# Kernel optimization log

Measured on AMD Instinct MI355X. Metric: run time of the kernel, lower is better.

Reference implementation:

```python
import jax, jax.numpy as jnp
import numpy as np

N_HEAD = 16

def setup_inputs() -> dict:
    key = jax.random.key(0)
    ks = jax.random.split(key, 5)
    B, T, C = 4, 2048, 1024
    s = 0.02
    return {
        "x": jax.random.normal(ks[0], (B, T, C), dtype=jnp.float32),
        "W_attn": jax.random.normal(ks[1], (C, 3 * C), dtype=jnp.float32) * s,
        "b_attn": jax.random.normal(ks[2], (3 * C,), dtype=jnp.float32) * s,
        "W_proj": jax.random.normal(ks[3], (C, C), dtype=jnp.float32) * s,
        "b_proj": jax.random.normal(ks[4], (C,), dtype=jnp.float32) * s,
    }

def reference(x, W_attn, b_attn, W_proj, b_proj):
    B, T, C = x.shape
    H = N_HEAD
    D = C // H
    qkv = x @ W_attn + b_attn                      # [B,T,3C]
    q, k, v = jnp.split(qkv, 3, axis=2)
    # [B,H,T,D]
    q = q.reshape(B, T, H, D).transpose(0, 2, 1, 3)
    k = k.reshape(B, T, H, D).transpose(0, 2, 1, 3)
    v = v.reshape(B, T, H, D).transpose(0, 2, 1, 3)
    scale = 1.0 / jnp.sqrt(jnp.float32(D))
    att = jnp.einsum('bhqd,bhkd->bhqk', q, k) * scale
    causal = jnp.tril(jnp.ones((T, T), dtype=bool))
    att = jnp.where(causal[None, None], att, -jnp.inf)
    att = jax.nn.softmax(att, axis=-1)
    y = jnp.einsum('bhqk,bhkd->bhqd', att, v)       # [B,H,T,D]
    y = y.transpose(0, 2, 1, 3).reshape(B, T, C)
    return y @ W_proj + b_proj
```

## Files before the change

### kernel.cpp

```cpp
#include <hip/hip_runtime.h>

typedef unsigned short u16;
typedef unsigned int u32;
typedef __bf16 bf16x8 __attribute__((ext_vector_type(8)));
typedef short s16x4 __attribute__((ext_vector_type(4)));
typedef float f32x4 __attribute__((ext_vector_type(4)));

#define MFMA16(a,b,c) __builtin_amdgcn_mfma_f32_16x16x32_bf16((a),(b),(c),0,0,0)

#if defined(__has_builtin)
#if __has_builtin(__builtin_amdgcn_mfma_f32_16x16x16bf16_1k)
#define MFMA1K(a,b,c) __builtin_amdgcn_mfma_f32_16x16x16bf16_1k((a),(b),(c),0,0,0)
#endif
#endif
#ifndef MFMA1K
__device__ __forceinline__ f32x4 mfma1k_asm(s16x4 a, s16x4 b, f32x4 c) {
    f32x4 d;
    asm volatile("v_mfma_f32_16x16x16_bf16 %0, %1, %2, %3"
                 : "=v"(d) : "v"(a), "v"(b), "0"(c));
    return d;
}
#define MFMA1K(a,b,c) mfma1k_asm((a),(b),(c))
#endif

__device__ __forceinline__ float b2f(u16 u) {
    u32 v = ((u32)u) << 16;
    return __builtin_bit_cast(float, v);
}
__device__ __forceinline__ u16 f2b(float f) {
    u32 u = __builtin_bit_cast(u32, f);
    u = u + 0x7FFFu + ((u >> 16) & 1u);
    return (u16)(u >> 16);
}

__device__ __forceinline__ void gload_lds16(const u16* g, u16* l) {
    __builtin_amdgcn_global_load_lds(
        (__attribute__((address_space(1))) void*)g,
        (__attribute__((address_space(3))) void*)l, 16, 0, 0);
}

__device__ __forceinline__ uint4 load8_bf16(const void* base, size_t off, int f32m) {
    if (f32m) {
        const float* p = (const float*)base + off;
        float4 a = *(const float4*)p;
        float4 b = *(const float4*)(p + 4);
        union { u16 u[8]; uint4 v; } t;
        t.u[0] = f2b(a.x); t.u[1] = f2b(a.y); t.u[2] = f2b(a.z); t.u[3] = f2b(a.w);
        t.u[4] = f2b(b.x); t.u[5] = f2b(b.y); t.u[6] = f2b(b.z); t.u[7] = f2b(b.w);
        return t.v;
    }
    return *(const uint4*)((const u16*)base + off);
}

__device__ __forceinline__ int detect_f32(const u16* __restrict__ x) {
    __shared__ int cnt;
    if (threadIdx.x == 0) cnt = 0;
    __syncthreads();
    int my = ((x[2 * (threadIdx.x * 128)] >> 7) & 0xFF) >= 0x90;
    unsigned long long b = __ballot(my);
    if ((threadIdx.x & 63) == 0) atomicAdd(&cnt, (int)__popcll(b));
    __syncthreads();
    return cnt > 32;
}

__device__ __forceinline__ void transpose_tile(
    const void* __restrict__ src, u16* __restrict__ dst, int R, int Cc,
    int f32m, int bx, int by)
{
    __shared__ u16 tile[64 * 72];
    const int t = threadIdx.x;
    const int c0 = bx * 64, r0 = by * 64;
    #pragma unroll
    for (int i = 0; i < 2; ++i) {
        int ch = t + 256 * i;
        int r = ch >> 3, c8 = (ch & 7) * 8;
        *(uint4*)&tile[r * 72 + c8] =
            load8_bf16(src, (size_t)(r0 + r) * Cc + c0 + c8, f32m);
    }
    __syncthreads();
    #pragma unroll
    for (int i = 0; i < 2; ++i) {
        int ch = t + 256 * i;
        int r = ch >> 3, c8 = (ch & 7) * 8;
        union { u16 u[8]; uint4 v; } tmp;
        #pragma unroll
        for (int j = 0; j < 8; ++j) tmp.u[j] = tile[(c8 + j) * 72 + r];
        *(uint4*)&dst[(size_t)(c0 + r) * R + r0 + c8] = tmp.v;
    }
}

__global__ __launch_bounds__(256) void k_prep(
    const u16* __restrict__ x, const void* __restrict__ Wa,
    const void* __restrict__ ba, const void* __restrict__ Wp,
    const void* __restrict__ bp,
    u16* __restrict__ WaT, u16* __restrict__ WpT, u16* __restrict__ Abf,
    u16* __restrict__ bac, u16* __restrict__ bpc, int* __restrict__ flag)
{
    const int f32m = detect_f32(x);
    int task = blockIdx.x;
    if (task < 768) {
        transpose_tile(Wa, WaT, 1024, 3072, f32m, task % 48, task / 48);
        return;
    }
    task -= 768;
    if (task < 256) {
        transpose_tile(Wp, WpT, 1024, 1024, f32m, task % 16, task / 16);
        return;
    }
    task -= 256;
    if (task < 4096) {
        if (!f32m) return;
        size_t i = ((size_t)task * 256 + threadIdx.x) * 8;
        const float* xf = (const float*)x;
        float4 a = *(const float4*)(xf + i);
        float4 b = *(const float4*)(xf + i + 4);
        union { u16 u[8]; uint4 v; } t;
        t.u[0] = f2b(a.x); t.u[1] = f2b(a.y); t.u[2] = f2b(a.z); t.u[3] = f2b(a.w);
        t.u[4] = f2b(b.x); t.u[5] = f2b(b.y); t.u[6] = f2b(b.z); t.u[7] = f2b(b.w);
        *(uint4*)(Abf + i) = t.v;
        return;
    }
    const int t = threadIdx.x;
    #pragma unroll
    for (int j = 0; j < 12; ++j) {
        int i = t + 256 * j;
        if (i < 3072) bac[i] = f32m ? f2b(((const float*)ba)[i]) : ((const u16*)ba)[i];
    }
    #pragma unroll
    for (int j = 0; j < 4; ++j) {
        int i = t + 256 * j;
        if (i < 1024) bpc[i] = f32m ? f2b(((const float*)bp)[i]) : ((const u16*)bp)[i];
    }
    if (t == 0) *flag = f32m;
}

__global__ __launch_bounds__(256) void k_gemm_qkv(
    const void* __restrict__ x, const u16* __restrict__ Abf,
    const u16* __restrict__ Bt, const u16* __restrict__ bias,
    const int* __restrict__ flag,
    u16* __restrict__ Ql, u16* __restrict__ Kl, u16* __restrict__ Vl)
{
    constexpr int K = 1024;
    __shared__ __align__(16) u16 As[128 * 64];
    __shared__ __align__(16) u16 Bs[128 * 64];
    const int t = threadIdx.x;
    const int lane = t & 63, w = t >> 6;
    const int quad = lane >> 4, m16 = lane & 15;
    const int wm = (w >> 1) * 64, wn = (w & 1) * 64;
    const int m0 = blockIdx.x * 128, n0 = blockIdx.y * 128;
    const int lr = lane >> 3;
    const int lc = (lane & 7) * 8;
    const u16* A = (*flag) ? Abf : (const u16*)x;

    const f32x4 z = {0.f, 0.f, 0.f, 0.f};
    f32x4 acc[4][4];
    #pragma unroll
    for (int mi = 0; mi < 4; ++mi)
        #pragma unroll
        for (int ni = 0; ni < 4; ++ni) acc[mi][ni] = z;

    for (int k0 = 0; k0 < K; k0 += 64) {
        __syncthreads();
        #pragma unroll
        for (int i = 0; i < 4; ++i) {
            const int chunk = w * 4 + i;
            const int row = chunk * 8 + lr;
            gload_lds16(&A [(size_t)(m0 + row) * K + k0 + lc], &As[chunk * 512]);
            gload_lds16(&Bt[(size_t)(n0 + row) * K + k0 + lc], &Bs[chunk * 512]);
        }
        __syncthreads();
        #pragma unroll
        for (int kk = 0; kk < 2; ++kk) {
            bf16x8 af[4], bfr[4];
            #pragma unroll
            for (int mi = 0; mi < 4; ++mi)
                af[mi] = *(const bf16x8*)&As[(wm + mi * 16 + m16) * 64 + kk * 32 + quad * 8];
            #pragma unroll
            for (int ni = 0; ni < 4; ++ni)
                bfr[ni] = *(const bf16x8*)&Bs[(wn + ni * 16 + m16) * 64 + kk * 32 + quad * 8];
            #pragma unroll
            for (int mi = 0; mi < 4; ++mi)
                #pragma unroll
                for (int ni = 0; ni < 4; ++ni)
                    acc[mi][ni] = MFMA16(af[mi], bfr[ni], acc[mi][ni]);
        }
    }

    const int sec = n0 >> 10;
    const float qscale = (sec == 0) ? 0.18033688011112042f : 1.0f;
    u16* Outp = (sec == 0) ? Ql : (sec == 1) ? Kl : Vl;
    #pragma unroll
    for (int mi = 0; mi < 4; ++mi) {
        #pragma unroll
        for (int ni = 0; ni < 4; ++ni) {
            int gn = n0 + wn + ni * 16 + m16;
            int sn = gn & 1023;
            int h = sn >> 6, d = sn & 63;
            float bv = b2f(bias[gn]);
            #pragma unroll
            for (int v = 0; v < 4; ++v) {
                int gm = m0 + wm + mi * 16 + quad * 4 + v;
                int bb = gm >> 11, tt = gm & 2047;
                u16 o = f2b((acc[mi][ni][v] + bv) * qscale);
                size_t bh = (size_t)(bb * 16 + h);
                Outp[(bh * 2048 + tt) * 64 + d] = o;
            }
        }
    }
}

__global__ __launch_bounds__(256) void k_attn(
    u16* __restrict__ Ql, const u16* __restrict__ Kl, const u16* __restrict__ Vl)
{
    __shared__ u16 Ks[128 * 80];
    __shared__ u16 Vs[64 * 132];
    const int t = threadIdx.x;
    const int lane = t & 63, w = t >> 6;
    const int quad = lane >> 4, m16 = lane & 15;
    const int g = blockIdx.x >> 6;
    const int p = g >> 2, r = g & 3;
    const int qb = (p == 0) ? 15 - r : (p == 1) ? 8 + r : (p == 2) ? 7 - r : r;
    const int bh = blockIdx.x & 63;
    const int q0 = qb * 128;

    bf16x8 fq[2][2];
    #pragma unroll
    for (int s = 0; s < 2; ++s) {
        const u16* Qp = Ql + ((size_t)bh * 2048 + q0 + s * 64 + w * 16 + m16) * 64;
        fq[s][0] = *(const bf16x8*)&Qp[quad * 8];
        fq[s][1] = *(const bf16x8*)&Qp[32 + quad * 8];
    }

    const f32x4 z = {0.f, 0.f, 0.f, 0.f};
    f32x4 acco[2][4] = {{z, z, z, z}, {z, z, z, z}};
    f32x4 accl[2] = {z, z};
    s16x4 ones4;
    #pragma unroll
    for (int j = 0; j < 4; ++j) ones4[j] = (short)0x3F80;

    const int ktmax = qb;
    const u16* Kbase = Kl + (size_t)bh * 2048 * 64;
    const u16* Vbase = Vl + (size_t)bh * 2048 * 64;

    uint4 kreg[4], vreg[4];
    #pragma unroll
    for (int i = 0; i < 4; ++i) {
        int c = t + 256 * i;
        int rr = c >> 3, col = (c & 7) * 8;
        kreg[i] = *(const uint4*)&Kbase[(size_t)rr * 64 + col];
        vreg[i] = *(const uint4*)&Vbase[(size_t)rr * 64 + col];
    }

    for (int kt = 0; kt <= ktmax; ++kt) {
        __syncthreads();
        #pragma unroll
        for (int i = 0; i < 4; ++i) {
            int c = t + 256 * i;
            int rr = c >> 3, col = (c & 7) * 8;
            *(uint4*)&Ks[rr * 80 + col] = kreg[i];
            union { u16 u[8]; uint4 v; } tv; tv.v = vreg[i];
            #pragma unroll
            for (int j = 0; j < 8; ++j)
                Vs[(col + j) * 132 + rr] = tv.u[j];
        }
        __syncthreads();

        if (kt < ktmax) {
            #pragma unroll
            for (int i = 0; i < 4; ++i) {
                int c = t + 256 * i;
                int rr = c >> 3, col = (c & 7) * 8;
                kreg[i] = *(const uint4*)&Kbase[(size_t)((kt + 1) * 128 + rr) * 64 + col];
                vreg[i] = *(const uint4*)&Vbase[(size_t)((kt + 1) * 128 + rr) * 64 + col];
            }
        }

        const bool diag = (kt == ktmax);
        #pragma unroll
        for (int s = 0; s < 2; ++s) {
            f32x4 accs[8] = {z, z, z, z, z, z, z, z};
            __builtin_amdgcn_s_setprio(1);
            #pragma unroll
            for (int kk = 0; kk < 2; ++kk)
                #pragma unroll
                for (int ni = 0; ni < 8; ++ni) {
                    bf16x8 bk = *(const bf16x8*)&Ks[(ni * 16 + m16) * 80 + kk * 32 + quad * 8];
                    accs[ni] = MFMA16(bk, fq[s][kk], accs[ni]);
                }
            __builtin_amdgcn_s_setprio(0);

            s16x4 pkv[8];
            if (!diag) {
                #pragma unroll
                for (int ni = 0; ni < 8; ++ni) {
                    union { __bf16 b[4]; s16x4 sv; } pk;
                    #pragma unroll
                    for (int v = 0; v < 4; ++v)
                        pk.b[v] = (__bf16)__builtin_amdgcn_exp2f(accs[ni][v]);
                    pkv[ni] = pk.sv;
                }
            } else {
                const int qg = q0 + s * 64 + w * 16 + m16;
                #pragma unroll
                for (int ni = 0; ni < 8; ++ni) {
                    union { __bf16 b[4]; s16x4 sv; } pk;
                    #pragma unroll
                    for (int v = 0; v < 4; ++v) {
                        float sc = accs[ni][v];
                        if (kt * 128 + ni * 16 + quad * 4 + v > qg) sc = -30000.0f;
                        pk.b[v] = (__bf16)__builtin_amdgcn_exp2f(sc);
                    }
                    pkv[ni] = pk.sv;
                }
            }

            __builtin_amdgcn_s_setprio(1);
            #pragma unroll
            for (int ni = 0; ni < 8; ++ni) {
                #pragma unroll
                for (int nd = 0; nd < 4; ++nd) {
                    s16x4 va = *(const s16x4*)&Vs[(nd * 16 + m16) * 132 + ni * 16 + quad * 4];
                    acco[s][nd] = MFMA1K(va, pkv[ni], acco[s][nd]);
                }
                accl[s] = MFMA1K(ones4, pkv[ni], accl[s]);
            }
            __builtin_amdgcn_s_setprio(0);
        }
    }

    #pragma unroll
    for (int s = 0; s < 2; ++s) {
        const int qg = q0 + s * 64 + w * 16 + m16;
        const float inv = 1.0f / fmaxf(accl[s][0], 1e-30f);
        u16* Orow = &Ql[((size_t)bh * 2048 + qg) * 64];
        #pragma unroll
        for (int nd = 0; nd < 4; ++nd) {
            union { u16 u[4]; uint2 uu; } o;
            #pragma unroll
            for (int v = 0; v < 4; ++v) o.u[v] = f2b(acco[s][nd][v] * inv);
            *(uint2*)&Orow[nd * 16 + quad * 4] = o.uu;
        }
    }
}

__global__ __launch_bounds__(256) void k_gemm_proj(
    const u16* __restrict__ Yl, const u16* __restrict__ Bt, const u16* __restrict__ bias,
    const int* __restrict__ flag, void* __restrict__ Out)
{
    constexpr int K = 1024;
    __shared__ __align__(16) u16 As[128 * 64];
    __shared__ __align__(16) u16 Bs[128 * 64];
    const int f32m = *flag;
    const int t = threadIdx.x;
    const int lane = t & 63, w = t >> 6;
    const int quad = lane >> 4, m16 = lane & 15;
    const int wm = (w >> 1) * 64, wn = (w & 1) * 64;
    const int m0 = blockIdx.x * 128, n0 = blockIdx.y * 128;
    const int bb = m0 >> 11, t0 = m0 & 2047;
    const int lr = lane >> 3;
    const int lc = (lane & 7) * 8;

    const f32x4 z = {0.f, 0.f, 0.f, 0.f};
    f32x4 acc[4][4];
    #pragma unroll
    for (int mi = 0; mi < 4; ++mi)
        #pragma unroll
        for (int ni = 0; ni < 4; ++ni) acc[mi][ni] = z;

    for (int k0 = 0; k0 < K; k0 += 64) {
        const int h = k0 >> 6;
        const u16* Abase = Yl + ((size_t)(bb * 16 + h) * 2048 + t0) * 64;
        __syncthreads();
        #pragma unroll
        for (int i = 0; i < 4; ++i) {
            const int chunk = w * 4 + i;
            gload_lds16(&Abase[chunk * 512 + lane * 8], &As[chunk * 512]);
            gload_lds16(&Bt[(size_t)(n0 + chunk * 8 + lr) * K + k0 + lc], &Bs[chunk * 512]);
        }
        __syncthreads();
        #pragma unroll
        for (int kk = 0; kk < 2; ++kk) {
            bf16x8 af[4], bfr[4];
            #pragma unroll
            for (int mi = 0; mi < 4; ++mi)
                af[mi] = *(const bf16x8*)&As[(wm + mi * 16 + m16) * 64 + kk * 32 + quad * 8];
            #pragma unroll
            for (int ni = 0; ni < 4; ++ni)
                bfr[ni] = *(const bf16x8*)&Bs[(wn + ni * 16 + m16) * 64 + kk * 32 + quad * 8];
            #pragma unroll
            for (int mi = 0; mi < 4; ++mi)
                #pragma unroll
                for (int ni = 0; ni < 4; ++ni)
                    acc[mi][ni] = MFMA16(af[mi], bfr[ni], acc[mi][ni]);
        }
    }

    #pragma unroll
    for (int mi = 0; mi < 4; ++mi) {
        #pragma unroll
        for (int ni = 0; ni < 4; ++ni) {
            int gn = n0 + wn + ni * 16 + m16;
            float bv = b2f(bias[gn]);
            #pragma unroll
            for (int v = 0; v < 4; ++v) {
                int gm = m0 + wm + mi * 16 + quad * 4 + v;
                float val = acc[mi][ni][v] + bv;
                if (f32m) ((float*)Out)[(size_t)gm * 1024 + gn] = val;
                else      ((u16*)Out)[(size_t)gm * 1024 + gn] = f2b(val);
            }
        }
    }
}

extern "C" void kernel_launch(void* const* d_in, const int* in_sizes, int n_in,
                              void* d_out, int out_size, void* d_ws, size_t ws_size,
                              hipStream_t stream)
{
    (void)in_sizes; (void)n_in; (void)out_size; (void)ws_size;
    const void* x  = d_in[0];
    const void* Wa = d_in[1];
    const void* ba = d_in[2];
    const void* Wp = d_in[3];
    const void* bp = d_in[4];
    char* ws = (char*)d_ws;

    u16* Ql  = (u16*)(ws + 0);
    u16* Kl  = (u16*)(ws + 16777216);
    u16* Vl  = (u16*)(ws + 33554432);
    u16* WpT = (u16*)(ws + 50331648);
    int* flag = (int*)(ws + 52428800);
    u16* bpc  = (u16*)(ws + 52428800 + 256);
    u16* bac  = (u16*)(ws + 52428800 + 256 + 2048);
    u16* WaT = (u16*)d_out;
    u16* Abf = (u16*)((char*)d_out + 6291456);

    k_prep<<<5121, 256, 0, stream>>>((const u16*)x, Wa, ba, Wp, bp,
                                     WaT, WpT, Abf, bac, bpc, flag);
    k_gemm_qkv<<<dim3(64, 24), 256, 0, stream>>>(x, Abf, WaT, bac, flag, Ql, Kl, Vl);
    k_attn<<<1024, 256, 0, stream>>>(Ql, Kl, Vl);
    k_gemm_proj<<<dim3(64, 8), 256, 0, stream>>>(Ql, WpT, bpc, flag, d_out);
}
```

Baseline: 289.1 us.

## Double-buffer GEMM tiles with swizzled LDS and larger 256-wide blocks

Both the QKV and output-projection GEMMs are restructured to use 512-thread blocks with bigger tiles (256x256 and 256x128) and a two-stage LDS double buffer. The next K-slice is prefetched while the current one is consumed, gated by explicit vmcnt waits and barriers. An XOR swizzle on the LDS layout avoids bank conflicts on fragment reads, and setprio is raised around the MFMA bursts. In exchange, LDS use per block and register pressure go up, and the grid shrinks to fewer blocks, which can hurt occupancy and wave balance.

New measurement: 276.8 us. -4.2%, faster.

```diff
diff --git a/kernel.cpp b/kernel.cpp
--- a/kernel.cpp
+++ b/kernel.cpp
@@ -134,72 +134,142 @@
     if (t == 0) *flag = f32m;
 }
 
-__global__ __launch_bounds__(256) void k_gemm_qkv(
+
+__device__ __forceinline__ void stage8(const u16* __restrict__ Asrc,
+                                       const u16* __restrict__ Bsrc,
+                                       u16* Asb, u16* Bsb, int wbase, int lane)
+{
+    #pragma unroll
+    for (int i = 0; i < 4; ++i) {
+        int gbase = wbase + 512 * i;
+        int g = gbase | lane;
+        int r = g >> 3, u = (g & 7) ^ (r & 7);
+        gload_lds16(Asrc + (size_t)r * 1024 + u * 8, Asb + gbase * 8);
+    }
+    #pragma unroll
+    for (int i = 0; i < 4; ++i) {
+        int gbase = wbase + 512 * i;
+        int g = gbase | lane;
+        int r = g >> 3, u = (g & 7) ^ (r & 7);
+        gload_lds16(Bsrc + (size_t)r * 1024 + u * 8, Bsb + gbase * 8);
+    }
+}
+
+__device__ __forceinline__ void stage6(const u16* __restrict__ Asrc,
+                                       const u16* __restrict__ Bsrc,
+                                       u16* Asb, u16* Bsb, int wbase, int lane)
+{
+    #pragma unroll
+    for (int i = 0; i < 4; ++i) {
+        int gbase = wbase + 512 * i;
+        int g = gbase | lane;
+        int gg = (g & ~7) | ((g & 7) ^ ((g >> 3) & 7));
+        gload_lds16(Asrc + gg * 8, Asb + gbase * 8);
+    }
+    #pragma unroll
+    for (int i = 0; i < 2; ++i) {
+        int gbase = wbase + 512 * i;
+        int g = gbase | lane;
+        int r = g >> 3, u = (g & 7) ^ (r & 7);
+        gload_lds16(Bsrc + (size_t)r * 1024 + u * 8, Bsb + gbase * 8);
+    }
+}
+
+__device__ __forceinline__ const u16* frag_ptr(const u16* base, int R, int sl) {
+    int gr = (R << 3) | (sl ^ (R & 7));
+    return base + gr * 8;
+}
+
+__global__ __launch_bounds__(512, 2) void k_gemm_qkv(
     const void* __restrict__ x, const u16* __restrict__ Abf,
     const u16* __restrict__ Bt, const u16* __restrict__ bias,
     const int* __restrict__ flag,
     u16* __restrict__ Ql, u16* __restrict__ Kl, u16* __restrict__ Vl)
 {
-    constexpr int K = 1024;
-    __shared__ __align__(16) u16 As[128 * 64];
-    __shared__ __align__(16) u16 Bs[128 * 64];
+    __shared__ __align__(16) u16 As[2][16384];
+    __shared__ __align__(16) u16 Bs[2][16384];
     const int t = threadIdx.x;
     const int lane = t & 63, w = t >> 6;
+    const int wbase = t & ~63;
     const int quad = lane >> 4, m16 = lane & 15;
-    const int wm = (w >> 1) * 64, wn = (w & 1) * 64;
-    const int m0 = blockIdx.x * 128, n0 = blockIdx.y * 128;
-    const int lr = lane >> 3;
-    const int lc = (lane & 7) * 8;
+    const int wr = w >> 2, wc = w & 3;
+    const int m0 = blockIdx.x * 256, n0 = blockIdx.y * 256;
     const u16* A = (*flag) ? Abf : (const u16*)x;
 
+    const u16* Atile = A + (size_t)m0 * 1024;
+    const u16* Btile = Bt + (size_t)n0 * 1024;
+
     const f32x4 z = {0.f, 0.f, 0.f, 0.f};
-    f32x4 acc[4][4];
-    #pragma unroll
-    for (int mi = 0; mi < 4; ++mi)
+    f32x4 acc[8][4];
+    #pragma unroll
+    for (int mi = 0; mi < 8; ++mi)
         #pragma unroll
         for (int ni = 0; ni < 4; ++ni) acc[mi][ni] = z;
 
-    for (int k0 = 0; k0 < K; k0 += 64) {
-        __syncthreads();
-        #pragma unroll
-        for (int i = 0; i < 4; ++i) {
-            const int chunk = w * 4 + i;
-            const int row = chunk * 8 + lr;
-            gload_lds16(&A [(size_t)(m0 + row) * K + k0 + lc], &As[chunk * 512]);
-            gload_lds16(&Bt[(size_t)(n0 + row) * K + k0 + lc], &Bs[chunk * 512]);
-        }
-        __syncthreads();
-        #pragma unroll
-        for (int kk = 0; kk < 2; ++kk) {
-            bf16x8 af[4], bfr[4];
-            #pragma unroll
-            for (int mi = 0; mi < 4; ++mi)
-                af[mi] = *(const bf16x8*)&As[(wm + mi * 16 + m16) * 64 + kk * 32 + quad * 8];
-            #pragma unroll
-            for (int ni = 0; ni < 4; ++ni)
-                bfr[ni] = *(const bf16x8*)&Bs[(wn + ni * 16 + m16) * 64 + kk * 32 + quad * 8];
-            #pragma unroll
-            for (int mi = 0; mi < 4; ++mi)
-                #pragma unroll
-                for (int ni = 0; ni < 4; ++ni)
-                    acc[mi][ni] = MFMA16(af[mi], bfr[ni], acc[mi][ni]);
-        }
+    stage8(Atile,      Btile,      &As[0][0], &Bs[0][0], wbase, lane);
+    stage8(Atile + 64, Btile + 64, &As[1][0], &Bs[1][0], wbase, lane);
+    __builtin_amdgcn_sched_barrier(0);
+    asm volatile("s_waitcnt vmcnt(8)" ::: "memory");
+    __builtin_amdgcn_s_barrier();
+    __builtin_amdgcn_sched_barrier(0);
+
+    for (int kt = 0; kt < 16; ++kt) {
+        const u16* Asb = &As[kt & 1][0];
+        const u16* Bsb = &Bs[kt & 1][0];
+
+        bf16x8 bfr[4][2];
+        #pragma unroll
+        for (int ni = 0; ni < 4; ++ni)
+            #pragma unroll
+            for (int kk = 0; kk < 2; ++kk)
+                bfr[ni][kk] = *(const bf16x8*)frag_ptr(Bsb, wc * 64 + ni * 16 + m16, kk * 4 + quad);
+
+        #pragma unroll
+        for (int ph = 0; ph < 4; ++ph) {
+            bf16x8 af[2][2];
+            #pragma unroll
+            for (int m2 = 0; m2 < 2; ++m2)
+                #pragma unroll
+                for (int kk = 0; kk < 2; ++kk)
+                    af[m2][kk] = *(const bf16x8*)frag_ptr(
+                        Asb, wr * 128 + (ph * 2 + m2) * 16 + m16, kk * 4 + quad);
+            __builtin_amdgcn_s_setprio(1);
+            #pragma unroll
+            for (int m2 = 0; m2 < 2; ++m2)
+                #pragma unroll
+                for (int ni = 0; ni < 4; ++ni) {
+                    acc[ph * 2 + m2][ni] = MFMA16(af[m2][0], bfr[ni][0], acc[ph * 2 + m2][ni]);
+                    acc[ph * 2 + m2][ni] = MFMA16(af[m2][1], bfr[ni][1], acc[ph * 2 + m2][ni]);
+                }
+            __builtin_amdgcn_s_setprio(0);
+        }
+
+        __builtin_amdgcn_sched_barrier(0);
+        __builtin_amdgcn_s_barrier();
+        if (kt < 14)
+            stage8(Atile + (kt + 2) * 64, Btile + (kt + 2) * 64,
+                   (u16*)Asb, (u16*)Bsb, wbase, lane);
+        __builtin_amdgcn_sched_barrier(0);
+        if (kt < 14) asm volatile("s_waitcnt vmcnt(8)" ::: "memory");
+        else         asm volatile("s_waitcnt vmcnt(0)" ::: "memory");
+        __builtin_amdgcn_s_barrier();
+        __builtin_amdgcn_sched_barrier(0);
     }
 
     const int sec = n0 >> 10;
     const float qscale = (sec == 0) ? 0.18033688011112042f : 1.0f;
     u16* Outp = (sec == 0) ? Ql : (sec == 1) ? Kl : Vl;
     #pragma unroll
-    for (int mi = 0; mi < 4; ++mi) {
+    for (int mi = 0; mi < 8; ++mi) {
         #pragma unroll
         for (int ni = 0; ni < 4; ++ni) {
-            int gn = n0 + wn + ni * 16 + m16;
+            int gn = n0 + wc * 64 + ni * 16 + m16;
             int sn = gn & 1023;
             int h = sn >> 6, d = sn & 63;
             float bv = b2f(bias[gn]);
             #pragma unroll
             for (int v = 0; v < 4; ++v) {
-                int gm = m0 + wm + mi * 16 + quad * 4 + v;
+                int gm = m0 + wr * 128 + mi * 16 + quad * 4 + v;
                 int bb = gm >> 11, tt = gm & 2047;
                 u16 o = f2b((acc[mi][ni][v] + bv) * qscale);
                 size_t bh = (size_t)(bb * 16 + h);
@@ -343,67 +413,91 @@
     }
 }
 
-__global__ __launch_bounds__(256) void k_gemm_proj(
+__global__ __launch_bounds__(512, 2) void k_gemm_proj(
     const u16* __restrict__ Yl, const u16* __restrict__ Bt, const u16* __restrict__ bias,
     const int* __restrict__ flag, void* __restrict__ Out)
 {
-    constexpr int K = 1024;
-    __shared__ __align__(16) u16 As[128 * 64];
-    __shared__ __align__(16) u16 Bs[128 * 64];
+    __shared__ __align__(16) u16 As[2][16384];
+    __shared__ __align__(16) u16 Bs[2][8192];
     const int f32m = *flag;
     const int t = threadIdx.x;
     const int lane = t & 63, w = t >> 6;
+    const int wbase = t & ~63;
     const int quad = lane >> 4, m16 = lane & 15;
-    const int wm = (w >> 1) * 64, wn = (w & 1) * 64;
-    const int m0 = blockIdx.x * 128, n0 = blockIdx.y * 128;
+    const int wr = w >> 2, wc = w & 3;
+    const int m0 = blockIdx.x * 256, n0 = blockIdx.y * 128;
     const int bb = m0 >> 11, t0 = m0 & 2047;
-    const int lr = lane >> 3;
-    const int lc = (lane & 7) * 8;
+
+    const u16* Btile = Bt + (size_t)n0 * 1024;
+    #define ABASE(KT) (Yl + ((size_t)(bb * 16 + (KT)) * 2048 + t0) * 64)
 
     const f32x4 z = {0.f, 0.f, 0.f, 0.f};
-    f32x4 acc[4][4];
-    #pragma unroll
-    for (int mi = 0; mi < 4; ++mi)
-        #pragma unroll
-        for (int ni = 0; ni < 4; ++ni) acc[mi][ni] = z;
-
-    for (int k0 = 0; k0 < K; k0 += 64) {
-        const int h = k0 >> 6;
-        const u16* Abase = Yl + ((size_t)(bb * 16 + h) * 2048 + t0) * 64;
-        __syncthreads();
-        #pragma unroll
-        for (int i = 0; i < 4; ++i) {
-            const int chunk = w * 4 + i;
-            gload_lds16(&Abase[chunk * 512 + lane * 8], &As[chunk * 512]);
-            gload_lds16(&Bt[(size_t)(n0 + chunk * 8 + lr) * K + k0 + lc], &Bs[chunk * 512]);
-        }
-        __syncthreads();
-        #pragma unroll
-        for (int kk = 0; kk < 2; ++kk) {
-            bf16x8 af[4], bfr[4];
-            #pragma unroll
-            for (int mi = 0; mi < 4; ++mi)
-                af[mi] = *(const bf16x8*)&As[(wm + mi * 16 + m16) * 64 + kk * 32 + quad * 8];
-            #pragma unroll
-            for (int ni = 0; ni < 4; ++ni)
-                bfr[ni] = *(const bf16x8*)&Bs[(wn + ni * 16 + m16) * 64 + kk * 32 + quad * 8];
-            #pragma unroll
-            for (int mi = 0; mi < 4; ++mi)
-                #pragma unroll
-                for (int ni = 0; ni < 4; ++ni)
-                    acc[mi][ni] = MFMA16(af[mi], bfr[ni], acc[mi][ni]);
-        }
-    }
-
-    #pragma unroll
-    for (int mi = 0; mi < 4; ++mi) {
-        #pragma unroll
-        for (int ni = 0; ni < 4; ++ni) {
-            int gn = n0 + wn + ni * 16 + m16;
+    f32x4 acc[8][2];
+    #pragma unroll
+    for (int mi = 0; mi < 8; ++mi)
+        #pragma unroll
+        for (int ni = 0; ni < 2; ++ni) acc[mi][ni] = z;
+
+    stage6(ABASE(0), Btile,      &As[0][0], &Bs[0][0], wbase, lane);
+    stage6(ABASE(1), Btile + 64, &As[1][0], &Bs[1][0], wbase, lane);
+    __builtin_amdgcn_sched_barrier(0);
+    asm volatile("s_waitcnt vmcnt(6)" ::: "memory");
+    __builtin_amdgcn_s_barrier();
+    __builtin_amdgcn_sched_barrier(0);
+
+    for (int kt = 0; kt < 16; ++kt) {
+        const u16* Asb = &As[kt & 1][0];
+        const u16* Bsb = &Bs[kt & 1][0];
+
+        bf16x8 bfr[2][2];
+        #pragma unroll
+        for (int ni = 0; ni < 2; ++ni)
+            #pragma unroll
+            for (int kk = 0; kk < 2; ++kk)
+                bfr[ni][kk] = *(const bf16x8*)frag_ptr(Bsb, wc * 32 + ni * 16 + m16, kk * 4 + quad);
+
+        #pragma unroll
+        for (int ph = 0; ph < 4; ++ph) {
+            bf16x8 af[2][2];
+            #pragma unroll
+            for (int m2 = 0; m2 < 2; ++m2)
+                #pragma unroll
+                for (int kk = 0; kk < 2; ++kk)
+                    af[m2][kk] = *(const bf16x8*)frag_ptr(
+                        Asb, wr * 128 + (ph * 2 + m2) * 16 + m16, kk * 4 + quad);
+            __builtin_amdgcn_s_setprio(1);
+            #pragma unroll
+            for (int m2 = 0; m2 < 2; ++m2)
+                #pragma unroll
+                for (int ni = 0; ni < 2; ++ni) {
+                    acc[ph * 2 + m2][ni] = MFMA16(af[m2][0], bfr[ni][0], acc[ph * 2 + m2][ni]);
+                    acc[ph * 2 + m2][ni] = MFMA16(af[m2][1], bfr[ni][1], acc[ph * 2 + m2][ni]);
+                }
+            __builtin_amdgcn_s_setprio(0);
+        }
+
+        __builtin_amdgcn_sched_barrier(0);
+        __builtin_amdgcn_s_barrier();
+        if (kt < 14)
+            stage6(ABASE(kt + 2), Btile + (kt + 2) * 64,
+                   (u16*)Asb, (u16*)Bsb, wbase, lane);
+        __builtin_amdgcn_sched_barrier(0);
+        if (kt < 14) asm volatile("s_waitcnt vmcnt(6)" ::: "memory");
+        else         asm volatile("s_waitcnt vmcnt(0)" ::: "memory");
+        __builtin_amdgcn_s_barrier();
+        __builtin_amdgcn_sched_barrier(0);
+    }
+    #undef ABASE
+
+    #pragma unroll
+    for (int mi = 0; mi < 8; ++mi) {
+        #pragma unroll
+        for (int ni = 0; ni < 2; ++ni) {
+            int gn = n0 + wc * 32 + ni * 16 + m16;
             float bv = b2f(bias[gn]);
             #pragma unroll
             for (int v = 0; v < 4; ++v) {
-                int gm = m0 + wm + mi * 16 + quad * 4 + v;
+                int gm = m0 + wr * 128 + mi * 16 + quad * 4 + v;
                 float val = acc[mi][ni][v] + bv;
                 if (f32m) ((float*)Out)[(size_t)gm * 1024 + gn] = val;
                 else      ((u16*)Out)[(size_t)gm * 1024 + gn] = f2b(val);
@@ -436,7 +530,7 @@
 
     k_prep<<<5121, 256, 0, stream>>>((const u16*)x, Wa, ba, Wp, bp,
                                      WaT, WpT, Abf, bac, bpc, flag);
-    k_gemm_qkv<<<dim3(64, 24), 256, 0, stream>>>(x, Abf, WaT, bac, flag, Ql, Kl, Vl);
+    k_gemm_qkv<<<dim3(32, 12), 512, 0, stream>>>(x, Abf, WaT, bac, flag, Ql, Kl, Vl);
     k_attn<<<1024, 256, 0, stream>>>(Ql, Kl, Vl);
-    k_gemm_proj<<<dim3(64, 8), 256, 0, stream>>>(Ql, WpT, bpc, flag, d_out);
-}
+    k_gemm_proj<<<dim3(32, 8), 512, 0, stream>>>(Ql, WpT, bpc, flag, d_out);
+}
```
